# Kernel tuning notes

Measured on AMD Instinct MI355X. Metric: run time of the kernel, lower is better.

The kernel has to match this reference:

```python
import jax, jax.numpy as jnp
import numpy as np
from jax.scipy.special import logsumexp

B, T = 64, 1024
NF, NH = 512, 512
NK = 500          # n_kcs (chains)
NS = 2            # n_states == n_outputs == 2


def setup_inputs() -> dict:
    key = jax.random.key(0)
    ks = jax.random.split(key, 8)
    return {
        "corr": jax.random.randint(ks[0], (B, T), 0, 2),
        "kc": jax.random.randint(ks[1], (B, T), 0, NK),
        "FM": jax.random.normal(ks[2], (B, T, NF), dtype=jnp.float32),
        "W1": jax.random.normal(ks[3], (NF, NH), jnp.float32) / np.sqrt(NF).astype(np.float32),
        "b1": jnp.zeros((NH,), jnp.float32),
        "W2": jax.random.normal(ks[4], (NH, 2), jnp.float32) / np.sqrt(NH).astype(np.float32),
        "b2": jnp.zeros((2,), jnp.float32),
        "trans_logits": jax.random.normal(ks[5], (NK, NS, NS), jnp.float32),
        "obs_logits": jax.random.normal(ks[6], (NK, NS, 2), jnp.float32),
        "init_logits": jax.random.normal(ks[7], (NK, NS), jnp.float32),
    }


def _bkt_forward(corr, kc, FM, W1, b1, W2, b2, trans_logits, obs_logits, init_logits):
    # MLP producing per-timestep observation logit features
    h = jnp.tanh(FM @ W1 + b1)                 # [B,T,NH]
    o = h @ W2 + b2                            # [B,T,2] (one per state)
    fv = jnp.stack([o, -o], axis=3)            # [B,T,NS,2] == cat((o, -o), dim=3)

    n_batch = corr.shape[0]
    bidx = jnp.arange(n_batch)
    log_t = jax.nn.log_softmax(trans_logits, axis=1)          # [NK,NS,NS], softmax over dim 1
    la0 = jnp.tile(jax.nn.log_softmax(init_logits, axis=1)[None], (n_batch, 1, 1))  # [B,NK,NS]

    def step(la_all, xs):
        y, c, fv_t = xs                         # y:[B] obs, c:[B] chain, fv_t:[B,NS,2]
        log_obs = jax.nn.log_softmax(obs_logits[c] + fv_t, axis=2)   # [B,NS,2]
        la = la_all[bidx, c]                    # [B,NS] gather current chain alpha
        log_py = logsumexp(log_obs + la[:, :, None], axis=1)         # [B,2]
        log_py = log_py - logsumexp(log_py, axis=1, keepdims=True)
        # emission prob of observed symbol per state: log_obs[b,:,y[b]]
        lp = jnp.take_along_axis(log_obs, y[:, None, None], axis=2)[..., 0]  # [B,NS]
        new_la = logsumexp(lp[:, None, :] + la[:, None, :] + log_t[c], axis=2)  # [B,NS]
        la_all = la_all.at[bidx, c].set(new_la)
        return la_all, log_py

    xs = (corr.T, kc.T, jnp.moveaxis(fv, 1, 0))   # time-major for scan
    _, outs = jax.lax.scan(step, la0, xs)         # outs: [T,B,2]
    return jnp.transpose(outs, (1, 0, 2))         # [B,T,2]


def reference(corr, kc, FM, W1, b1, W2, b2, trans_logits, obs_logits, init_logits):
    return _bkt_forward(corr, kc, FM, W1, b1, W2, b2, trans_logits, obs_logits, init_logits)
```

## Files before the change

kernel.cpp:

```cpp
#include <hip/hip_runtime.h>
#include <hip/hip_bf16.h>
#include <stdint.h>

typedef unsigned short u16;
typedef __bf16 bf16x8 __attribute__((ext_vector_type(8)));
typedef float floatx4 __attribute__((ext_vector_type(4)));

#define B_SZ 64
#define T_SZ 1024
#define NK 500

__device__ __forceinline__ u16 f2bf(float f) {
    union { float f; uint32_t u; } v; v.f = f;
    uint32_t u = v.u;
    u += 0x7FFFu + ((u >> 16) & 1u);
    return (u16)(u >> 16);
}

__device__ __forceinline__ float exp2_hw(float x) { return __builtin_amdgcn_exp2f(x); }
__device__ __forceinline__ float log2_hw(float x) { return __builtin_amdgcn_logf(x); }

__device__ __forceinline__ float lse2(float a, float b) {
    float m = fmaxf(a, b);
    float d = fabsf(a - b);
    return fmaf(0.6931471805599453f,
                log2_hw(1.0f + exp2_hw(-d * 1.4426950408889634f)), m);
}

__global__ __launch_bounds__(256) void transpose_cvt(const float* __restrict__ in,
                                                     u16* __restrict__ out) {
    __shared__ float tile[32][33];
    int tx = threadIdx.x, ty = threadIdx.y;
    int x = blockIdx.x * 32 + tx;
    int y0 = blockIdx.y * 32 + ty;
    for (int i = 0; i < 32; i += 8)
        tile[ty + i][tx] = in[(size_t)(y0 + i) * 512 + x];
    __syncthreads();
    int x2 = blockIdx.y * 32 + tx;
    int y2 = blockIdx.x * 32 + ty;
    for (int i = 0; i < 32; i += 8)
        out[(size_t)(y2 + i) * 512 + x2] = f2bf(tile[tx][ty + i]);
}

__global__ __launch_bounds__(512, 4) void mlp_fused(
    const float* __restrict__ FM, const u16* __restrict__ W1T,
    const float* __restrict__ b1, const float* __restrict__ W2,
    const float* __restrict__ b2, float* __restrict__ o_buf) {

    __shared__ __align__(16) u16 ldsA[64 * 512];
    __shared__ float ldsO[64][8][2];

    const int tid  = threadIdx.x;
    const int w    = tid >> 6;
    const int lane = tid & 63;
    const int col  = lane & 15;
    const int g    = lane >> 4;
    const size_t row0 = (size_t)blockIdx.x * 64;

#pragma unroll
    for (int i = 0; i < 8; ++i) {
        int flat = i * 512 + tid;
        int row  = flat >> 6;
        int k8   = flat & 63;
        const float* src = FM + (row0 + row) * 512 + k8 * 8;
        float4 f0 = ((const float4*)src)[0];
        float4 f1 = ((const float4*)src)[1];
        union { uint4 v; u16 s[8]; } p;
        p.s[0] = f2bf(f0.x); p.s[1] = f2bf(f0.y);
        p.s[2] = f2bf(f0.z); p.s[3] = f2bf(f0.w);
        p.s[4] = f2bf(f1.x); p.s[5] = f2bf(f1.y);
        p.s[6] = f2bf(f1.z); p.s[7] = f2bf(f1.w);
        int sw = k8 ^ (row & 7);
        *(uint4*)(ldsA + row * 512 + sw * 8) = p.v;
    }
    __syncthreads();

    const u16* bbase = W1T + (size_t)(w * 64 + col) * 512 + g * 8;

    floatx4 acc[4][4];
    floatx4 zero = {0.f, 0.f, 0.f, 0.f};
#pragma unroll
    for (int mi = 0; mi < 4; mi++)
#pragma unroll
        for (int ni = 0; ni < 4; ni++) acc[mi][ni] = zero;

    bf16x8 bA[4], bB[4];
#pragma unroll
    for (int ni = 0; ni < 4; ni++)
        bA[ni] = *(const bf16x8*)(bbase + ni * 16 * 512);

    for (int ks2 = 0; ks2 < 16; ks2 += 2) {
#pragma unroll
        for (int ni = 0; ni < 4; ni++)
            bB[ni] = *(const bf16x8*)(bbase + ni * 16 * 512 + (ks2 + 1) * 32);
        {
            bf16x8 afr[4];
            int sw = (ks2 * 4 + g) ^ (col & 7);
#pragma unroll
            for (int mi = 0; mi < 4; mi++)
                afr[mi] = *(const bf16x8*)(ldsA + (mi * 16 + col) * 512 + sw * 8);
#pragma unroll
            for (int mi = 0; mi < 4; mi++)
#pragma unroll
                for (int ni = 0; ni < 4; ni++)
                    acc[mi][ni] = __builtin_amdgcn_mfma_f32_16x16x32_bf16(
                        afr[mi], bA[ni], acc[mi][ni], 0, 0, 0);
        }
        int ksn = (ks2 + 2) & 15;
#pragma unroll
        for (int ni = 0; ni < 4; ni++)
            bA[ni] = *(const bf16x8*)(bbase + ni * 16 * 512 + ksn * 32);
        {
            bf16x8 afr[4];
            int sw = ((ks2 + 1) * 4 + g) ^ (col & 7);
#pragma unroll
            for (int mi = 0; mi < 4; mi++)
                afr[mi] = *(const bf16x8*)(ldsA + (mi * 16 + col) * 512 + sw * 8);
#pragma unroll
            for (int mi = 0; mi < 4; mi++)
#pragma unroll
                for (int ni = 0; ni < 4; ni++)
                    acc[mi][ni] = __builtin_amdgcn_mfma_f32_16x16x32_bf16(
                        afr[mi], bB[ni], acc[mi][ni], 0, 0, 0);
        }
    }

    float po[4][4][2];
#pragma unroll
    for (int mi = 0; mi < 4; mi++)
#pragma unroll
        for (int r = 0; r < 4; r++) { po[mi][r][0] = 0.f; po[mi][r][1] = 0.f; }

#pragma unroll
    for (int ni = 0; ni < 4; ni++) {
        int n = w * 64 + ni * 16 + col;
        float b1f = b1[n];
        float w20 = W2[2 * n], w21 = W2[2 * n + 1];
#pragma unroll
        for (int mi = 0; mi < 4; mi++)
#pragma unroll
            for (int r = 0; r < 4; r++) {
                float x = acc[mi][ni][r] + b1f;
                float ax = fabsf(x);
                float e = exp2_hw(-2.885390082f * ax);
                float t = (1.f - e) / (1.f + e);
                float h = copysignf(t, x);
                po[mi][r][0] += h * w20;
                po[mi][r][1] += h * w21;
            }
    }

#pragma unroll
    for (int mi = 0; mi < 4; mi++)
#pragma unroll
        for (int r = 0; r < 4; r++)
#pragma unroll
            for (int j = 0; j < 2; j++) {
                float v = po[mi][r][j];
                v += __shfl_xor(v, 1, 64);
                v += __shfl_xor(v, 2, 64);
                v += __shfl_xor(v, 4, 64);
                v += __shfl_xor(v, 8, 64);
                po[mi][r][j] = v;
            }
    if (col == 0) {
#pragma unroll
        for (int mi = 0; mi < 4; mi++)
#pragma unroll
            for (int r = 0; r < 4; r++) {
                int row = mi * 16 + g * 4 + r;
                ldsO[row][w][0] = po[mi][r][0];
                ldsO[row][w][1] = po[mi][r][1];
            }
    }
    __syncthreads();
    if (tid < 128) {
        int row = tid >> 1, j = tid & 1;
        float v = ldsO[row][0][j] + ldsO[row][1][j]
                + ldsO[row][2][j] + ldsO[row][3][j]
                + ldsO[row][4][j] + ldsO[row][5][j]
                + ldsO[row][6][j] + ldsO[row][7][j] + b2[j];
        o_buf[(row0 + row) * 2 + j] = v;
    }
}

__global__ __launch_bounds__(64) void bkt_scan(
    const int* __restrict__ corr, const int* __restrict__ kc,
    const float* __restrict__ trans_logits,
    const float* __restrict__ obs_logits,
    const float* __restrict__ init_logits,
    const float* __restrict__ o_buf,
    float* __restrict__ out) {

    __shared__ int s_kc[T_SZ];
    __shared__ int s_corr[T_SZ];
    __shared__ float2 s_o[T_SZ];
    const int b = blockIdx.x >> 3;
    const int g = blockIdx.x & 7;
    const int lane = threadIdx.x;

#pragma unroll
    for (int i = 0; i < 4; ++i) {
        int t4 = i * 64 + lane;
        ((int4*)s_kc)[t4]   = ((const int4*)(kc + b * T_SZ))[t4];
        ((int4*)s_corr)[t4] = ((const int4*)(corr + b * T_SZ))[t4];
    }
#pragma unroll
    for (int i = 0; i < 8; ++i) {
        int t4 = i * 64 + lane;
        ((float4*)s_o)[t4] = ((const float4*)(o_buf + (size_t)b * T_SZ * 2))[t4];
    }
    __syncthreads();

    const int c  = g * 64 + lane;
    const int cp = c < NK ? c : NK - 1;

    float ob00 = obs_logits[cp * 4 + 0], ob01 = obs_logits[cp * 4 + 1];
    float ob10 = obs_logits[cp * 4 + 2], ob11 = obs_logits[cp * 4 + 3];
    float tr00 = trans_logits[cp * 4 + 0], tr01 = trans_logits[cp * 4 + 1];
    float tr10 = trans_logits[cp * 4 + 2], tr11 = trans_logits[cp * 4 + 3];
    float n0 = lse2(tr00, tr10), n1 = lse2(tr01, tr11);
    float lt00 = tr00 - n0, lt01 = tr01 - n1;
    float lt10 = tr10 - n0, lt11 = tr11 - n1;
    float i0 = init_logits[cp * 2], i1 = init_logits[cp * 2 + 1];
    float nli = lse2(i0, i1);
    float la0 = i0 - nli, la1 = i1 - nli;

    for (int w16 = 0; w16 < 16; ++w16) {
        int tl = w16 * 64 + lane;
        unsigned long long mask = __ballot((s_kc[tl] >> 6) == g);
        while (mask) {
            int tz = __builtin_ctzll(mask);
            mask &= mask - 1;
            int t = w16 * 64 + tz;
            int kct = s_kc[t];
            if (c == kct) {
                float o0 = s_o[t].x, o1 = s_o[t].y;
                float x00 = ob00 + o0, x01 = ob01 - o0;
                float x10 = ob10 + o1, x11 = ob11 - o1;
                float d0 = lse2(x00, x01), d1 = lse2(x10, x11);
                float lo00 = x00 - d0, lo01 = x01 - d0;
                float lo10 = x10 - d1, lo11 = x11 - d1;
                float py0 = lse2(lo00 + la0, lo10 + la1);
                float py1 = lse2(lo01 + la0, lo11 + la1);
                float pn = lse2(py0, py1);
                ((float2*)out)[(size_t)b * T_SZ + t] = make_float2(py0 - pn, py1 - pn);
                float lp0 = s_corr[t] ? lo01 : lo00;
                float lp1 = s_corr[t] ? lo11 : lo10;
                float t0 = lp0 + la0, t1 = lp1 + la1;
                float nla0 = lse2(t0 + lt00, t1 + lt01);
                float nla1 = lse2(t0 + lt10, t1 + lt11);
                la0 = nla0; la1 = nla1;
            }
        }
    }
}

extern "C" void kernel_launch(void* const* d_in, const int* in_sizes, int n_in,
                              void* d_out, int out_size, void* d_ws, size_t ws_size,
                              hipStream_t stream) {
    const int*   corr = (const int*)d_in[0];
    const int*   kc   = (const int*)d_in[1];
    const float* FM   = (const float*)d_in[2];
    const float* W1   = (const float*)d_in[3];
    const float* b1   = (const float*)d_in[4];
    const float* W2   = (const float*)d_in[5];
    const float* b2   = (const float*)d_in[6];
    const float* trans_logits = (const float*)d_in[7];
    const float* obs_logits   = (const float*)d_in[8];
    const float* init_logits  = (const float*)d_in[9];
    float* out = (float*)d_out;

    u16*   w1t   = (u16*)d_ws;
    float* o_buf = (float*)((char*)d_ws + 512 * 512 * 2);

    transpose_cvt<<<dim3(16, 16), dim3(32, 8), 0, stream>>>(W1, w1t);
    mlp_fused<<<1024, 512, 0, stream>>>(FM, w1t, b1, W2, b2, o_buf);
    bkt_scan<<<B_SZ * 8, 64, 0, stream>>>(corr, kc, trans_logits, obs_logits,
                                          init_logits, o_buf, out);
}
```

Baseline: 320.2 us.

## Pre-pack W1 into MFMA fragment order and defer BKT output computation

Result: slower. 337.6 us (+5.4%).

```diff
diff --git a/kernel.cpp b/kernel.cpp
--- a/kernel.cpp
+++ b/kernel.cpp
@@ -27,23 +27,24 @@
                 log2_hw(1.0f + exp2_hw(-d * 1.4426950408889634f)), m);
 }
 
-__global__ __launch_bounds__(256) void transpose_cvt(const float* __restrict__ in,
-                                                     u16* __restrict__ out) {
-    __shared__ float tile[32][33];
-    int tx = threadIdx.x, ty = threadIdx.y;
-    int x = blockIdx.x * 32 + tx;
-    int y0 = blockIdx.y * 32 + ty;
-    for (int i = 0; i < 32; i += 8)
-        tile[ty + i][tx] = in[(size_t)(y0 + i) * 512 + x];
-    __syncthreads();
-    int x2 = blockIdx.y * 32 + tx;
-    int y2 = blockIdx.x * 32 + ty;
-    for (int i = 0; i < 32; i += 8)
-        out[(size_t)(y2 + i) * 512 + x2] = f2bf(tile[tx][ty + i]);
+__global__ __launch_bounds__(256) void pack_w1(const float* __restrict__ in,
+                                               u16* __restrict__ out) {
+    int idx = blockIdx.x * 256 + threadIdx.x;
+    int l     = idx & 63;
+    int ks    = (idx >> 6) & 15;
+    int ntile = idx >> 10;
+    int col = l & 15, gg = l >> 4;
+    int n = ntile * 16 + col;
+    int kbase = ks * 32 + gg * 8;
+    union { uint4 v; u16 s[8]; } p;
+#pragma unroll
+    for (int j = 0; j < 8; ++j)
+        p.s[j] = f2bf(in[(size_t)(kbase + j) * 512 + n]);
+    *(uint4*)(out + (size_t)idx * 8) = p.v;
 }
 
 __global__ __launch_bounds__(512, 4) void mlp_fused(
-    const float* __restrict__ FM, const u16* __restrict__ W1T,
+    const float* __restrict__ FM, const u16* __restrict__ W1P,
     const float* __restrict__ b1, const float* __restrict__ W2,
     const float* __restrict__ b2, float* __restrict__ o_buf) {
 
@@ -75,7 +76,7 @@
     }
     __syncthreads();
 
-    const u16* bbase = W1T + (size_t)(w * 64 + col) * 512 + g * 8;
+    const u16* bbase = W1P + ((size_t)(w * 4 * 16) * 64 + lane) * 8;
 
     floatx4 acc[4][4];
     floatx4 zero = {0.f, 0.f, 0.f, 0.f};
@@ -87,12 +88,12 @@
     bf16x8 bA[4], bB[4];
 #pragma unroll
     for (int ni = 0; ni < 4; ni++)
-        bA[ni] = *(const bf16x8*)(bbase + ni * 16 * 512);
+        bA[ni] = *(const bf16x8*)(bbase + (ni * 16 + 0) * 512);
 
     for (int ks2 = 0; ks2 < 16; ks2 += 2) {
 #pragma unroll
         for (int ni = 0; ni < 4; ni++)
-            bB[ni] = *(const bf16x8*)(bbase + ni * 16 * 512 + (ks2 + 1) * 32);
+            bB[ni] = *(const bf16x8*)(bbase + (ni * 16 + ks2 + 1) * 512);
         {
             bf16x8 afr[4];
             int sw = (ks2 * 4 + g) ^ (col & 7);
@@ -109,7 +110,7 @@
         int ksn = (ks2 + 2) & 15;
 #pragma unroll
         for (int ni = 0; ni < 4; ni++)
-            bA[ni] = *(const bf16x8*)(bbase + ni * 16 * 512 + ksn * 32);
+            bA[ni] = *(const bf16x8*)(bbase + (ni * 16 + ksn) * 512);
         {
             bf16x8 afr[4];
             int sw = ((ks2 + 1) * 4 + g) ^ (col & 7);
@@ -195,6 +196,8 @@
     __shared__ int s_kc[T_SZ];
     __shared__ int s_corr[T_SZ];
     __shared__ float2 s_o[T_SZ];
+    __shared__ short s_idx[T_SZ];
+    __shared__ float2 s_la[T_SZ];
     const int b = blockIdx.x >> 3;
     const int g = blockIdx.x & 7;
     const int lane = threadIdx.x;
@@ -215,17 +218,18 @@
     const int c  = g * 64 + lane;
     const int cp = c < NK ? c : NK - 1;
 
-    float ob00 = obs_logits[cp * 4 + 0], ob01 = obs_logits[cp * 4 + 1];
-    float ob10 = obs_logits[cp * 4 + 2], ob11 = obs_logits[cp * 4 + 3];
     float tr00 = trans_logits[cp * 4 + 0], tr01 = trans_logits[cp * 4 + 1];
     float tr10 = trans_logits[cp * 4 + 2], tr11 = trans_logits[cp * 4 + 3];
     float n0 = lse2(tr00, tr10), n1 = lse2(tr01, tr11);
     float lt00 = tr00 - n0, lt01 = tr01 - n1;
     float lt10 = tr10 - n0, lt11 = tr11 - n1;
+    float ob00 = obs_logits[cp * 4 + 0], ob01 = obs_logits[cp * 4 + 1];
+    float ob10 = obs_logits[cp * 4 + 2], ob11 = obs_logits[cp * 4 + 3];
     float i0 = init_logits[cp * 2], i1 = init_logits[cp * 2 + 1];
     float nli = lse2(i0, i1);
     float la0 = i0 - nli, la1 = i1 - nli;
 
+    int cnt = 0;
     for (int w16 = 0; w16 < 16; ++w16) {
         int tl = w16 * 64 + lane;
         unsigned long long mask = __ballot((s_kc[tl] >> 6) == g);
@@ -234,25 +238,44 @@
             mask &= mask - 1;
             int t = w16 * 64 + tz;
             int kct = s_kc[t];
+            float pla0 = __shfl(la0, kct & 63, 64);
+            float pla1 = __shfl(la1, kct & 63, 64);
+            if (lane == 0) {
+                s_idx[cnt] = (short)t;
+                s_la[cnt]  = make_float2(pla0, pla1);
+            }
+            cnt++;
             if (c == kct) {
                 float o0 = s_o[t].x, o1 = s_o[t].y;
                 float x00 = ob00 + o0, x01 = ob01 - o0;
                 float x10 = ob10 + o1, x11 = ob11 - o1;
                 float d0 = lse2(x00, x01), d1 = lse2(x10, x11);
-                float lo00 = x00 - d0, lo01 = x01 - d0;
-                float lo10 = x10 - d1, lo11 = x11 - d1;
-                float py0 = lse2(lo00 + la0, lo10 + la1);
-                float py1 = lse2(lo01 + la0, lo11 + la1);
-                float pn = lse2(py0, py1);
-                ((float2*)out)[(size_t)b * T_SZ + t] = make_float2(py0 - pn, py1 - pn);
-                float lp0 = s_corr[t] ? lo01 : lo00;
-                float lp1 = s_corr[t] ? lo11 : lo10;
+                float lp0 = (s_corr[t] ? x01 : x00) - d0;
+                float lp1 = (s_corr[t] ? x11 : x10) - d1;
                 float t0 = lp0 + la0, t1 = lp1 + la1;
                 float nla0 = lse2(t0 + lt00, t1 + lt01);
                 float nla1 = lse2(t0 + lt10, t1 + lt11);
                 la0 = nla0; la1 = nla1;
             }
         }
+    }
+
+    __builtin_amdgcn_s_waitcnt(0);
+    for (int j = lane; j < cnt; j += 64) {
+        int t = s_idx[j];
+        int kct = s_kc[t];
+        float4 ol = ((const float4*)obs_logits)[kct];
+        float la0p = s_la[j].x, la1p = s_la[j].y;
+        float o0 = s_o[t].x, o1 = s_o[t].y;
+        float x00 = ol.x + o0, x01 = ol.y - o0;
+        float x10 = ol.z + o1, x11 = ol.w - o1;
+        float d0 = lse2(x00, x01), d1 = lse2(x10, x11);
+        float lo00 = x00 - d0, lo01 = x01 - d0;
+        float lo10 = x10 - d1, lo11 = x11 - d1;
+        float py0 = lse2(lo00 + la0p, lo10 + la1p);
+        float py1 = lse2(lo01 + la0p, lo11 + la1p);
+        float pn = lse2(py0, py1);
+        ((float2*)out)[(size_t)b * T_SZ + t] = make_float2(py0 - pn, py1 - pn);
     }
 }
 
@@ -271,11 +294,11 @@
     const float* init_logits  = (const float*)d_in[9];
     float* out = (float*)d_out;
 
-    u16*   w1t   = (u16*)d_ws;
+    u16*   w1p   = (u16*)d_ws;
     float* o_buf = (float*)((char*)d_ws + 512 * 512 * 2);
 
-    transpose_cvt<<<dim3(16, 16), dim3(32, 8), 0, stream>>>(W1, w1t);
-    mlp_fused<<<1024, 512, 0, stream>>>(FM, w1t, b1, W2, b2, o_buf);
+    pack_w1<<<128, 256, 0, stream>>>(W1, w1p);
+    mlp_fused<<<1024, 512, 0, stream>>>(FM, w1p, b1, W2, b2, o_buf);
     bkt_scan<<<B_SZ * 8, 64, 0, stream>>>(corr, kc, trans_logits, obs_logits,
                                           init_logits, o_buf, out);
 }
```
